# Kernel tuning notes

Measured on AMD Instinct MI355X. Metric: run time of the kernel, lower is better.

The kernel has to match this reference:

```python
import jax, jax.numpy as jnp
import numpy as np

B, N, V, D = 4, 1024, 20000, 512
DEPTH, H, DH, W = 6, 8, 64, 512
NB = N // W
NS = 512               # num_state_vectors
PM = D // 4            # dynamic pos-bias MLP width
XL_LAYERS = (4, 5)     # 0-indexed (config layers 5, 6)
REC_LAYER = 3          # 0-indexed (config layer 4)
QK_RMS = {3, 4, 5}     # recurrent + xl layers use qk rmsnorm
QK_SCALE = 8.0
FF = 4 * D


def _ln(x, g, eps=1e-5):
    mu = x.mean(-1, keepdims=True)
    var = ((x - mu) ** 2).mean(-1, keepdims=True)
    return (x - mu) * jax.lax.rsqrt(var + eps) * g


def _l2norm(x):
    return x * jax.lax.rsqrt((x * x).sum(-1, keepdims=True) + 1e-12)


def _pos_bias(pos_w1, pos_b1, pos_w2, pos_b2, pos_w3, pos_b3):
    # MLP over scalar relative distance -> per-head bias table [W, H]
    d = jnp.arange(W, dtype=jnp.float32)[:, None]
    h = jax.nn.silu(d @ pos_w1 + pos_b1)
    h = jax.nn.silu(h @ pos_w2 + pos_b2)
    table = h @ pos_w3 + pos_b3                       # [W, H]
    i = jnp.arange(W)[:, None]
    j = jnp.arange(2 * W)[None, :]
    rel = jnp.abs(i + W - j)                          # distance to key in [prev|cur] window
    win = (j > i) & (j <= i + W)                      # causal sliding window of width W
    pb = table[jnp.where(win, rel, 0)]                # [W, 2W, H]
    return jnp.transpose(pb, (2, 0, 1)), win          # [H, W, 2W], [W, 2W]


def setup_inputs() -> dict:
    key = jax.random.key(0)
    ks = iter(jax.random.split(key, 64))
    w = lambda shape, s=0.02: jax.random.normal(next(ks), shape, jnp.float32) * s
    return dict(
        x=jax.random.randint(next(ks), (B, N), 0, V, jnp.int32),
        tok_emb=w((V, D)),
        pos_w1=w((1, PM)), pos_b1=jnp.zeros((PM,), jnp.float32),
        pos_w2=w((PM, PM)), pos_b2=jnp.zeros((PM,), jnp.float32),
        pos_w3=w((PM, H)), pos_b3=jnp.zeros((H,), jnp.float32),
        ln_g=jnp.ones((DEPTH, D), jnp.float32),
        Wq=w((DEPTH, D, H * DH)), Wk=w((DEPTH, D, H * DH)),
        Wv=w((DEPTH, D, H * DH)), Wo=w((DEPTH, H * DH, D)),
        q_scale=jnp.ones((DEPTH, DH), jnp.float32),
        k_scale=jnp.ones((DEPTH, DH), jnp.float32),
        Wo_state=w((H * DH, D)),
        state_norm_g=jnp.ones((D,), jnp.float32),
        Wq2s=w((D, H * DH)), Ws2q=w((D, H * DH)), Ws2kv=w((D, 2 * DH)),
        W_state_out=w((H * DH, D)),
        ema_beta=jnp.zeros((D,), jnp.float32),
        ff_g=jnp.ones((DEPTH, D), jnp.float32),
        ff_w1=w((DEPTH, D, FF)), ff_b1=jnp.zeros((DEPTH, FF), jnp.float32),
        ff_w2=w((DEPTH, FF, D)), ff_b2=jnp.zeros((DEPTH, D), jnp.float32),
        final_g=jnp.ones((D,), jnp.float32),
        W_logits=w((D, V)),
        xl_mem_k=jax.random.normal(next(ks), (len(XL_LAYERS), B, W, H, DH), jnp.float32),
        xl_mem_v=jax.random.normal(next(ks), (len(XL_LAYERS), B, W, H, DH), jnp.float32),
        states=jax.random.normal(next(ks), (B, NS, D), jnp.float32),
    )


def reference(x, tok_emb, pos_w1, pos_b1, pos_w2, pos_b2, pos_w3, pos_b3,
              ln_g, Wq, Wk, Wv, Wo, q_scale, k_scale, Wo_state,
              state_norm_g, Wq2s, Ws2q, Ws2kv, W_state_out, ema_beta,
              ff_g, ff_w1, ff_b1, ff_w2, ff_b2, final_g, W_logits,
              xl_mem_k, xl_mem_v, states):
    pb, win = _pos_bias(pos_w1, pos_b1, pos_w2, pos_b2, pos_w3, pos_b3)
    j = jnp.arange(2 * W)
    no_mem = win & (j[None, :] >= W)                  # first block of a non-xl layer has no memory
    scale_dh = DH ** -0.5
    # enhanced recurrence: rotate the xl memory stack one layer down
    xk = jnp.roll(xl_mem_k, -1, axis=0)
    xv = jnp.roll(xl_mem_v, -1, axis=0)

    hstate = tok_emb[x]                               # [B, N, D]
    next_xl_k, next_xl_v = [], []
    next_states = states
    xl_idx = 0
    for l in range(DEPTH):
        xn = _ln(hstate, ln_g[l])
        q = (xn @ Wq[l]).reshape(B, N, H, DH)
        k = (xn @ Wk[l]).reshape(B, N, H, DH)
        v = (xn @ Wv[l]).reshape(B, N, H, DH)
        if l in QK_RMS:
            q = _l2norm(q) * q_scale[l]
            k = _l2norm(k) * k_scale[l]
            scale = QK_SCALE
        else:
            scale = scale_dh
        qb = q.reshape(B, NB, W, H, DH)
        kb = k.reshape(B, NB, W, H, DH)
        vb = v.reshape(B, NB, W, H, DH)
        is_xl = l in XL_LAYERS
        if is_xl:
            mem_k, mem_v = xk[xl_idx], xv[xl_idx]     # [B, W, H, DH] kv carried from prior call
            valid = jnp.stack([win] * NB)             # [NB, W, 2W]
        else:
            mem_k = jnp.zeros_like(kb[:, 0])
            mem_v = jnp.zeros_like(vb[:, 0])
            valid = jnp.stack([no_mem] + [win] * (NB - 1))
        # each block attends to [previous block | current block]
        pk = jnp.concatenate([mem_k[:, None], kb[:, :-1]], axis=1)
        pv = jnp.concatenate([mem_v[:, None], vb[:, :-1]], axis=1)
        kcat = jnp.concatenate([pk, kb], axis=2)      # [B, NB, 2W, H, DH]
        vcat = jnp.concatenate([pv, vb], axis=2)
        scores = jnp.einsum('bnihd,bnjhd->bnhij', qb * scale, kcat) + pb[None, None]
        scores = jnp.where(valid[None, :, None], scores, -1e9)
        attn = jax.nn.softmax(scores, axis=-1)
        out = jnp.einsum('bnhij,bnjhd->bnihd', attn, vcat).reshape(B, N, H * DH)
        branch = out @ Wo[l]
        if l == REC_LAYER:
            # recurrent state vectors: scan over blocks carrying states
            xn_blk = jnp.moveaxis(xn.reshape(B, NB, W, D), 1, 0)   # [NB, B, W, D]
            kb_s = jnp.moveaxis(kb, 1, 0)
            vb_s = jnp.moveaxis(vb, 1, 0)

            def step(st, inp):
                xb, kblk, vblk = inp
                sn = _ln(st, state_norm_g)
                s_k, s_v = jnp.split(sn @ Ws2kv, 2, axis=-1)       # single-head kv [B, NS, DH]
                # block tokens cross-attend to states
                q2s = (xb @ Wq2s).reshape(B, W, H, DH) * scale_dh
                a = jax.nn.softmax(jnp.einsum('bihd,bjd->bhij', q2s, s_k), -1)
                t_out = jnp.einsum('bhij,bjd->bihd', a, s_v).reshape(B, W, H * DH)
                # states attend to [states | block tokens]
                sq = (sn @ Ws2q).reshape(B, NS, H, DH) * scale_dh
                kc = jnp.concatenate([jnp.broadcast_to(s_k[:, :, None], (B, NS, H, DH)), kblk], axis=1)
                vc = jnp.concatenate([jnp.broadcast_to(s_v[:, :, None], (B, NS, H, DH)), vblk], axis=1)
                a2 = jax.nn.softmax(jnp.einsum('bihd,bjhd->bhij', sq, kc), -1)
                s_out = jnp.einsum('bhij,bjhd->bihd', a2, vc).reshape(B, NS, H * DH) @ W_state_out
                decay = jax.nn.sigmoid(ema_beta)
                return decay * st + (1.0 - decay) * s_out, t_out

            next_states, t_outs = jax.lax.scan(step, states, (xn_blk, kb_s, vb_s))
            to_state = jnp.moveaxis(t_outs, 0, 1).reshape(B, N, H * DH)
            branch = branch + to_state @ Wo_state
        hstate = hstate + branch
        if is_xl:
            next_xl_k.append(kb[:, -1])
            next_xl_v.append(vb[:, -1])
            xl_idx += 1
        fn = _ln(hstate, ff_g[l])
        hstate = hstate + (jax.nn.gelu(fn @ ff_w1[l] + ff_b1[l]) @ ff_w2[l] + ff_b2[l])

    logits = _ln(hstate, final_g) @ W_logits          # [B, N, V]
    return logits, jnp.stack(next_xl_k), jnp.stack(next_xl_v), next_states
```

## Files before the change

### kernel.cpp

```cpp
#include <hip/hip_runtime.h>
#include <math.h>


typedef __attribute__((ext_vector_type(8))) _Float16 f16x8;
typedef __attribute__((ext_vector_type(4))) float f32x4;

__device__ __forceinline__ ushort f2h(float f){
  _Float16 h = (_Float16)f;
  return *reinterpret_cast<ushort*>(&h);
}
__device__ __forceinline__ uint pkh2(float a, float b){
  return (uint)f2h(a) | ((uint)f2h(b)<<16);
}

__global__ __launch_bounds__(256)
void k_prep(const float* __restrict__ src, ushort* __restrict__ dh,
            int K, int N, int Npad, long zStride){
  __shared__ float tile[32][33];
  int z = blockIdx.z;
  src += (size_t)z*K*N;
  dh  += (size_t)z*zStride;
  int n0 = blockIdx.x*32, k0 = blockIdx.y*32;
  int tx = threadIdx.x&31, ty = threadIdx.x>>5;
#pragma unroll
  for (int i=0;i<4;i++){
    int kk = k0 + ty + i*8, nn = n0 + tx;
    tile[ty+i*8][tx] = (nn < N) ? src[(size_t)kk*N + nn] : 0.f;
  }
  __syncthreads();
#pragma unroll
  for (int i=0;i<4;i++){
    int nn = n0 + ty + i*8, kk = k0 + tx;
    dh[(size_t)nn*K + kk] = f2h(tile[tx][ty+i*8]);
  }
}

__global__ __launch_bounds__(256)
void k_vtrans(const float* __restrict__ src, ushort* __restrict__ dst,
              long sB, int sR, int sMH, long dB, long dH, int NK){
  __shared__ float tile[64][65];
  int kc = blockIdx.x, h = blockIdx.y, b = blockIdx.z;
  int t = threadIdx.x;
  int key = t>>2, doff = (t&3)*16;
  const float* sp = src + (size_t)b*sB + (size_t)(kc*64+key)*sR + (sMH? h*64:0) + doff;
#pragma unroll
  for (int u=0;u<4;u++){
    float4 v = *reinterpret_cast<const float4*>(sp + u*4);
    tile[key][doff+u*4+0]=v.x; tile[key][doff+u*4+1]=v.y;
    tile[key][doff+u*4+2]=v.z; tile[key][doff+u*4+3]=v.w;
  }
  __syncthreads();
  int d = t>>2, kf = (t&3)*16;
  ushort* dp = dst + (size_t)b*dB + (size_t)h*dH + (size_t)d*NK + kc*64 + kf;
  ushort tmp[16];
#pragma unroll
  for (int u=0;u<16;u++) tmp[u] = f2h(tile[kf+u][d]);
  uint4 o0 = make_uint4((uint)tmp[0]|((uint)tmp[1]<<16), (uint)tmp[2]|((uint)tmp[3]<<16),
                        (uint)tmp[4]|((uint)tmp[5]<<16), (uint)tmp[6]|((uint)tmp[7]<<16));
  uint4 o1 = make_uint4((uint)tmp[8]|((uint)tmp[9]<<16), (uint)tmp[10]|((uint)tmp[11]<<16),
                        (uint)tmp[12]|((uint)tmp[13]<<16),(uint)tmp[14]|((uint)tmp[15]<<16));
  *reinterpret_cast<uint4*>(dp)   = o0;
  *reinterpret_cast<uint4*>(dp+8) = o1;
}

__global__ __launch_bounds__(256)
void k_vtrans16(const ushort* __restrict__ src, ushort* __restrict__ dst,
                long sB, int sR, long dB, int NK){
  __shared__ ushort tile[64][72];
  int kc = blockIdx.x, b = blockIdx.z;
  int t = threadIdx.x;
  int key = t>>2, doff = (t&3)*16;
  const ushort* sp = src + (size_t)b*sB + (size_t)(kc*64+key)*sR + doff;
  *reinterpret_cast<uint4*>(&tile[key][doff])   = *reinterpret_cast<const uint4*>(sp);
  *reinterpret_cast<uint4*>(&tile[key][doff+8]) = *reinterpret_cast<const uint4*>(sp+8);
  __syncthreads();
  int d = t>>2, kf = (t&3)*16;
  ushort* dp = dst + (size_t)b*dB + (size_t)d*NK + kc*64 + kf;
  ushort tmp[16];
#pragma unroll
  for (int u=0;u<16;u++) tmp[u] = tile[kf+u][d];
  uint4 o0 = make_uint4((uint)tmp[0]|((uint)tmp[1]<<16), (uint)tmp[2]|((uint)tmp[3]<<16),
                        (uint)tmp[4]|((uint)tmp[5]<<16), (uint)tmp[6]|((uint)tmp[7]<<16));
  uint4 o1 = make_uint4((uint)tmp[8]|((uint)tmp[9]<<16), (uint)tmp[10]|((uint)tmp[11]<<16),
                        (uint)tmp[12]|((uint)tmp[13]<<16),(uint)tmp[14]|((uint)tmp[15]<<16));
  *reinterpret_cast<uint4*>(dp)   = o0;
  *reinterpret_cast<uint4*>(dp+8) = o1;
}

__global__ void k_cvt(ushort* __restrict__ dst, const float* __restrict__ src, int n2){
  int idx = blockIdx.x*blockDim.x + threadIdx.x;
  if (idx >= n2) return;
  reinterpret_cast<uint*>(dst)[idx] = pkh2(src[2*idx], src[2*idx+1]);
}

__global__ void k_embed(const int* __restrict__ x, const float* __restrict__ emb,
                        float* __restrict__ h, int total4){
  int idx = blockIdx.x*blockDim.x + threadIdx.x;
  if (idx >= total4) return;
  int row = idx >> 7;
  int c4  = idx & 127;
  int tok = x[row];
  reinterpret_cast<float4*>(h)[idx] =
      reinterpret_cast<const float4*>(emb)[(size_t)tok*128 + c4];
}

__global__ void k_postable(const float* __restrict__ w1, const float* __restrict__ b1,
                           const float* __restrict__ w2, const float* __restrict__ b2,
                           const float* __restrict__ w3, const float* __restrict__ b3,
                           float* __restrict__ table){
  __shared__ float h1[128];
  __shared__ float h2[128];
  int d = blockIdx.x, t = threadIdx.x;
  float a = (float)d * w1[t] + b1[t];
  h1[t] = a / (1.f + __expf(-a));
  __syncthreads();
  float acc = b2[t];
  for (int p=0;p<128;p++) acc += h1[p]*w2[p*128+t];
  h2[t] = acc / (1.f + __expf(-acc));
  __syncthreads();
  if (t < 8){
    float acc2 = b3[t];
    for (int p=0;p<128;p++) acc2 += h2[p]*w3[p*8+t];
    table[d*8+t] = acc2;
  }
}

__global__ void k_ln(const float* __restrict__ x, const float* __restrict__ g,
                     ushort* __restrict__ y16){
  int row = blockIdx.x;
  int t = threadIdx.x;
  float2 v = reinterpret_cast<const float2*>(x + (size_t)row*512)[t];
  float s = v.x+v.y, ss = v.x*v.x+v.y*v.y;
  for (int o=32;o;o>>=1){ s += __shfl_down(s,o); ss += __shfl_down(ss,o); }
  __shared__ float ls[4], lss[4];
  __shared__ float smu, srs;
  int wid = t>>6;
  if ((t&63)==0){ ls[wid]=s; lss[wid]=ss; }
  __syncthreads();
  if (t==0){
    float S=ls[0]+ls[1]+ls[2]+ls[3], SS=lss[0]+lss[1]+lss[2]+lss[3];
    float mu = S*(1.f/512.f);
    float var = SS*(1.f/512.f) - mu*mu;
    smu = mu; srs = rsqrtf(var + 1e-5f);
  }
  __syncthreads();
  float mu=smu, rs=srs;
  float2 gg = reinterpret_cast<const float2*>(g)[t];
  float ya = (v.x-mu)*rs*gg.x, yb = (v.y-mu)*rs*gg.y;
  *reinterpret_cast<uint*>(&y16[(size_t)row*512 + 2*t]) = pkh2(ya, yb);
}

__device__ __forceinline__ float geluf(float x){
  float u = 1.5957691216f*(x + 0.044715f*x*x*x);
  return x / (1.f + __expf(-u));
}

template<int ACC, int EPI, int OUT16>
__global__ __launch_bounds__(256)
void k_gemmh(const ushort* __restrict__ A, const ushort* __restrict__ Bt,
             const float* __restrict__ bias, float* __restrict__ C,
             ushort* __restrict__ C16, int M, int N, int K){
  __shared__ ushort As[128][68];
  __shared__ ushort Bs[128][68];
  const int t = threadIdx.x;
  const int m0 = blockIdx.x*128, n0 = blockIdx.y*128;
  const int w = t>>6, lane = t&63;
  const int wm = (w>>1)*64, wn = (w&1)*64;
  const int fr = lane&15, fg = lane>>4;
  const int srow = t>>1, sko = (t&1)*32;

  f32x4 acc[4][4];
#pragma unroll
  for (int i=0;i<4;i++)
#pragma unroll
    for (int j=0;j<4;j++){ acc[i][j][0]=0.f; acc[i][j][1]=0.f; acc[i][j][2]=0.f; acc[i][j][3]=0.f; }

  const ushort* ap = A  + (size_t)(m0+srow)*K + sko;
  const ushort* bp = Bt + (size_t)(n0+srow)*K + sko;

  for (int k0=0; k0<K; k0+=64){
    uint4 av[4], bv[4];
#pragma unroll
    for (int u=0;u<4;u++){
      av[u] = *reinterpret_cast<const uint4*>(ap + k0 + u*8);
      bv[u] = *reinterpret_cast<const uint4*>(bp + k0 + u*8);
    }
#pragma unroll
    for (int u=0;u<4;u++){
      *reinterpret_cast<uint4*>(&As[srow][sko+u*8]) = av[u];
      *reinterpret_cast<uint4*>(&Bs[srow][sko+u*8]) = bv[u];
    }
    __syncthreads();
#pragma unroll
    for (int kk=0;kk<2;kk++){
      f16x8 af[4], bf[4];
#pragma unroll
      for (int mi=0;mi<4;mi++)
        af[mi] = *reinterpret_cast<const f16x8*>(&As[wm+mi*16+fr][kk*32+fg*8]);
#pragma unroll
      for (int nj=0;nj<4;nj++)
        bf[nj] = *reinterpret_cast<const f16x8*>(&Bs[wn+nj*16+fr][kk*32+fg*8]);
#pragma unroll
      for (int mi=0;mi<4;mi++)
#pragma unroll
        for (int nj=0;nj<4;nj++)
          acc[mi][nj] = __builtin_amdgcn_mfma_f32_16x16x32_f16(af[mi], bf[nj], acc[mi][nj], 0,0,0);
    }
    __syncthreads();
  }
#pragma unroll
  for (int mi=0;mi<4;mi++){
#pragma unroll
    for (int r=0;r<4;r++){
      int row = m0 + wm + mi*16 + fg*4 + r;
#pragma unroll
      for (int nj=0;nj<4;nj++){
        int col = n0 + wn + nj*16 + fr;
        if (col < N){
          float val = acc[mi][nj][r];
          if (bias) val += bias[col];
          if (EPI==1) val = geluf(val);
          if (OUT16){
            C16[(size_t)row*N + col] = f2h(val);
          } else {
            if (ACC) C[(size_t)row*N + col] += val; else C[(size_t)row*N + col] = val;
          }
        }
      }
    }
  }
}

template<int REMAP>
__global__ __launch_bounds__(256)
void k_gemmqk(const ushort* __restrict__ A, const ushort* __restrict__ Bt,
              ushort* __restrict__ C1h, int ld1, int N1,
              ushort* __restrict__ C2h, int ld2,
              const float* __restrict__ qsc, const float* __restrict__ ksc,
              float* __restrict__ xlk,
              int nb, int M, int N, int K){
  __shared__ ushort As[128][68];
  __shared__ ushort Bs[128][68];
  const int t = threadIdx.x;
  const int m0 = blockIdx.x*128, n0 = blockIdx.y*128;
  const int w = t>>6, lane = t&63;
  const int wm = (w>>1)*64, wn = (w&1)*64;
  const int fr = lane&15, fg = lane>>4;
  const int srow = t>>1, sko = (t&1)*32;

  f32x4 acc[4][4];
#pragma unroll
  for (int i=0;i<4;i++)
#pragma unroll
    for (int j=0;j<4;j++){ acc[i][j][0]=0.f; acc[i][j][1]=0.f; acc[i][j][2]=0.f; acc[i][j][3]=0.f; }

  int mrow = m0 + srow;
  int arow = REMAP ? ((mrow>>9)*1024 + nb*512 + (mrow&511)) : mrow;
  const ushort* ap = A  + (size_t)arow*K + sko;
  const ushort* bp = Bt + (size_t)(n0+srow)*K + sko;

  for (int k0=0; k0<K; k0+=64){
    uint4 av[4], bv[4];
#pragma unroll
    for (int u=0;u<4;u++){
      av[u] = *reinterpret_cast<const uint4*>(ap + k0 + u*8);
      bv[u] = *reinterpret_cast<const uint4*>(bp + k0 + u*8);
    }
#pragma unroll
    for (int u=0;u<4;u++){
      *reinterpret_cast<uint4*>(&As[srow][sko+u*8]) = av[u];
      *reinterpret_cast<uint4*>(&Bs[srow][sko+u*8]) = bv[u];
    }
    __syncthreads();
#pragma unroll
    for (int kk=0;kk<2;kk++){
      f16x8 af[4], bf[4];
#pragma unroll
      for (int mi=0;mi<4;mi++)
        af[mi] = *reinterpret_cast<const f16x8*>(&As[wm+mi*16+fr][kk*32+fg*8]);
#pragma unroll
      for (int nj=0;nj<4;nj++)
        bf[nj] = *reinterpret_cast<const f16x8*>(&Bs[wn+nj*16+fr][kk*32+fg*8]);
#pragma unroll
      for (int mi=0;mi<4;mi++)
#pragma unroll
        for (int nj=0;nj<4;nj++)
          acc[mi][nj] = __builtin_amdgcn_mfma_f32_16x16x32_f16(af[mi], bf[nj], acc[mi][nj], 0,0,0);
    }
    __syncthreads();
  }
#pragma unroll
  for (int mi=0;mi<4;mi++){
#pragma unroll
    for (int r=0;r<4;r++){
      int row = m0 + wm + mi*16 + fg*4 + r;
      float vals[4];
#pragma unroll
      for (int nj=0;nj<4;nj++) vals[nj] = acc[mi][nj][r];
      if (qsc){
        float ss = vals[0]*vals[0]+vals[1]*vals[1]+vals[2]*vals[2]+vals[3]*vals[3];
        ss += __shfl_xor(ss,1);
        ss += __shfl_xor(ss,2);
        ss += __shfl_xor(ss,4);
        ss += __shfl_xor(ss,8);
        float rs = rsqrtf(ss + 1e-12f);
        const float* sc = ((n0+wn) < N1) ? qsc : ksc;
#pragma unroll
        for (int nj=0;nj<4;nj++) vals[nj] = vals[nj]*rs*sc[nj*16+fr];
      }
#pragma unroll
      for (int nj=0;nj<4;nj++){
        int col = n0 + wn + nj*16 + fr;
        float val = vals[nj];
        if (col < N1){
          C1h[(size_t)row*ld1 + col] = f2h(val);
        } else if (col < N){
          if (C2h) C2h[(size_t)row*ld2 + (col-N1)] = f2h(val);
          if (xlk && (row&1023) >= 512)
            xlk[((size_t)(row>>10)*512 + (row&1023) - 512)*512 + (col-N1)] = val;
        }
      }
    }
  }
}

template<int ACC, int EPI, int OUT16, int VT>
__global__ __launch_bounds__(256)
void k_gemmh64(const ushort* __restrict__ A, const ushort* __restrict__ Bt,
               const float* __restrict__ bias, float* __restrict__ C,
               ushort* __restrict__ C16, ushort* __restrict__ vT,
               float* __restrict__ xlv, int M, int N, int K){
  __shared__ ushort As[64][68];
  __shared__ ushort Bs[128][68];
  const int t = threadIdx.x;
  const int m0 = blockIdx.x*64, n0 = blockIdx.y*128;
  const int w = t>>6, lane = t&63;
  const int wm = (w>>1)*32, wn = (w&1)*64;
  const int fr = lane&15, fg = lane>>4;
  const int srowA = t>>2, skoA = (t&3)*16;
  const int srowB = t>>1, skoB = (t&1)*32;

  f32x4 acc[2][4];
#pragma unroll
  for (int i=0;i<2;i++)
#pragma unroll
    for (int j=0;j<4;j++){ acc[i][j][0]=0.f; acc[i][j][1]=0.f; acc[i][j][2]=0.f; acc[i][j][3]=0.f; }

  const ushort* ap = A  + (size_t)(m0+srowA)*K + skoA;
  const ushort* bp = Bt + (size_t)(n0+srowB)*K + skoB;

  for (int k0=0; k0<K; k0+=64){
    uint4 a0 = *reinterpret_cast<const uint4*>(ap + k0);
    uint4 a1 = *reinterpret_cast<const uint4*>(ap + k0 + 8);
    uint4 b0 = *reinterpret_cast<const uint4*>(bp + k0);
    uint4 b1 = *reinterpret_cast<const uint4*>(bp + k0 + 8);
    uint4 b2 = *reinterpret_cast<const uint4*>(bp + k0 + 16);
    uint4 b3 = *reinterpret_cast<const uint4*>(bp + k0 + 24);
    *reinterpret_cast<uint4*>(&As[srowA][skoA])    = a0;
    *reinterpret_cast<uint4*>(&As[srowA][skoA+8])  = a1;
    *reinterpret_cast<uint4*>(&Bs[srowB][skoB])    = b0;
    *reinterpret_cast<uint4*>(&Bs[srowB][skoB+8])  = b1;
    *reinterpret_cast<uint4*>(&Bs[srowB][skoB+16]) = b2;
    *reinterpret_cast<uint4*>(&Bs[srowB][skoB+24]) = b3;
    __syncthreads();
#pragma unroll
    for (int kk=0;kk<2;kk++){
      f16x8 af[2], bf[4];
#pragma unroll
      for (int mi=0;mi<2;mi++)
        af[mi] = *reinterpret_cast<const f16x8*>(&As[wm+mi*16+fr][kk*32+fg*8]);
#pragma unroll
      for (int nj=0;nj<4;nj++)
        bf[nj] = *reinterpret_cast<const f16x8*>(&Bs[wn+nj*16+fr][kk*32+fg*8]);
#pragma unroll
      for (int mi=0;mi<2;mi++)
#pragma unroll
        for (int nj=0;nj<4;nj++)
          acc[mi][nj] = __builtin_amdgcn_mfma_f32_16x16x32_f16(af[mi], bf[nj], acc[mi][nj], 0,0,0);
    }
    __syncthreads();
  }
#pragma unroll
  for (int mi=0;mi<2;mi++){
#pragma unroll
    for (int r=0;r<4;r++){
      int row = m0 + wm + mi*16 + fg*4 + r;
#pragma unroll
      for (int nj=0;nj<4;nj++){
        int col = n0 + wn + nj*16 + fr;
        if (col < N){
          float val = acc[mi][nj][r];
          if (EPI==2){
            size_t idx = (size_t)row*N + col;
            float old = C[idx];
            float dec = 1.f/(1.f+__expf(-bias[col]));
            C[idx] = dec*old + (1.f-dec)*val;
          } else {
            if (bias) val += bias[col];
            if (EPI==1) val = geluf(val);
            if (OUT16){
              if (C16) C16[(size_t)row*N + col] = f2h(val);
            } else if (C){
              if (ACC) C[(size_t)row*N + col] += val; else C[(size_t)row*N + col] = val;
            }
            if (VT && xlv && (row&1023) >= 512)
              xlv[((size_t)(row>>10)*512 + (row&1023) - 512)*512 + col] = val;
          }
        }
      }
    }
  }
  if (VT){
#pragma unroll
    for (int mi=0;mi<2;mi++)
#pragma unroll
      for (int r=0;r<4;r++)
#pragma unroll
        for (int nj=0;nj<4;nj++)
          Bs[wn+nj*16+fr][wm+mi*16+fg*4+r] = f2h(acc[mi][nj][r]);
    __syncthreads();
    int c = t>>1, half = t&1;
    int hh = (n0+c)>>6, dd = (n0+c)&63;
    int bb = m0>>10, posb = m0&1023;
    ushort* dp = vT + (size_t)bb*524288 + (size_t)hh*65536 + (size_t)dd*1024 + posb + half*32;
#pragma unroll
    for (int u=0;u<4;u++)
      *reinterpret_cast<uint4*>(dp + u*8) = *reinterpret_cast<const uint4*>(&Bs[c][half*32 + u*8]);
  }
}

__global__ __launch_bounds__(256)
void k_attn_win(const ushort* __restrict__ q16, const ushort* __restrict__ k16,
                const ushort* __restrict__ vTb,
                const ushort* __restrict__ xlK, const ushort* __restrict__ xlVT,
                int isxl, ushort* __restrict__ O, float scale,
                const float* __restrict__ table){
  __shared__ ushort Qs[64][72];
  __shared__ ushort Ks[64][72];
  __shared__ ushort Vs[64][72];
  __shared__ ushort Pw[4][16][72];
  __shared__ float tcol[512];
  const int b = blockIdx.z, h = blockIdx.y;
  const int nb = blockIdx.x>>3, qt = blockIdx.x&7;
  const int t = threadIdx.x, w = t>>6, lane = t&63;
  const int fr = lane&15, fg = lane>>4;
  tcol[t]     = table[t*8 + h];
  tcol[t+256] = table[(t+256)*8 + h];

  const ushort* Q  = q16 + (size_t)nb*262144;
  const ushort* K1 = k16 + (size_t)nb*262144;
  const ushort* V1 = vTb + (size_t)nb*512;
  ushort* Op = O + (size_t)nb*262144;
  const int has_mem = (nb==1) || isxl;
  const ushort* K0; long k0B; const ushort* V0; long vt0B, vt0H; int vt0D;
  if (nb==1){ K0=k16; k0B=524288; V0=vTb; vt0B=524288; vt0H=65536; vt0D=1024; }
  else if (isxl){ K0=xlK; k0B=262144; V0=xlVT; vt0B=262144; vt0H=32768; vt0D=512; }
  else { K0=k16; k0B=524288; V0=vTb; vt0B=524288; vt0H=65536; vt0D=1024; }

  {
    int qrow = t>>2, doff = (t&3)*16;
    const ushort* qp = Q + (size_t)b*524288 + (size_t)(qt*64+qrow)*512 + h*64 + doff;
    *reinterpret_cast<uint4*>(&Qs[qrow][doff])   = *reinterpret_cast<const uint4*>(qp);
    *reinterpret_cast<uint4*>(&Qs[qrow][doff+8]) = *reinterpret_cast<const uint4*>(qp+8);
  }
  __syncthreads();
  f16x8 aq[2];
  aq[0] = *reinterpret_cast<const f16x8*>(&Qs[w*16+fr][fg*8]);
  aq[1] = *reinterpret_cast<const f16x8*>(&Qs[w*16+fr][32+fg*8]);

  f32x4 so[4];
#pragma unroll
  for (int dt=0;dt<4;dt++){ so[dt][0]=0.f; so[dt][1]=0.f; so[dt][2]=0.f; so[dt][3]=0.f; }
  float m[4] = {-1e30f,-1e30f,-1e30f,-1e30f};
  float lsum[4] = {0.f,0.f,0.f,0.f};

  const int srow = t>>2, sdo = (t&3)*16;
  const int vd = t>>2,   vkf = (t&3)*16;

  int jt0 = has_mem ? qt : 8;
  int jt1 = qt + 8; if (jt1 > 15) jt1 = 15;

  for (int jt=jt0; jt<=jt1; jt++){
    {
      int key = jt*64 + srow;
      const ushort* kp;
      if (key < 512) kp = K0 + (size_t)b*k0B + (size_t)key*512 + h*64 + sdo;
      else           kp = K1 + (size_t)b*524288 + (size_t)(key-512)*512 + h*64 + sdo;
      *reinterpret_cast<uint4*>(&Ks[srow][sdo])   = *reinterpret_cast<const uint4*>(kp);
      *reinterpret_cast<uint4*>(&Ks[srow][sdo+8]) = *reinterpret_cast<const uint4*>(kp+8);
    }
    {
      const ushort* vp;
      if (jt*64 < 512) vp = V0 + (size_t)b*vt0B + (size_t)h*vt0H + (size_t)vd*vt0D + jt*64 + vkf;
      else             vp = V1 + (size_t)b*524288 + (size_t)h*65536 + (size_t)vd*1024 + (jt*64-512) + vkf;
      *reinterpret_cast<uint4*>(&Vs[vd][vkf])   = *reinterpret_cast<const uint4*>(vp);
      *reinterpret_cast<uint4*>(&Vs[vd][vkf+8]) = *reinterpret_cast<const uint4*>(vp+8);
    }
    __syncthreads();
    f32x4 sacc[4];
#pragma unroll
    for (int kt=0;kt<4;kt++){ sacc[kt][0]=0.f; sacc[kt][1]=0.f; sacc[kt][2]=0.f; sacc[kt][3]=0.f; }
#pragma unroll
    for (int ks=0;ks<2;ks++){
#pragma unroll
      for (int kt=0;kt<4;kt++){
        f16x8 bf = *reinterpret_cast<const f16x8*>(&Ks[kt*16+fr][ks*32+fg*8]);
        sacc[kt] = __builtin_amdgcn_mfma_f32_16x16x32_f16(aq[ks], bf, sacc[kt], 0,0,0);
      }
    }
#pragma unroll
    for (int r=0;r<4;r++){
      float sv[4];
      int ia = qt*64 + w*16 + fg*4 + r;
#pragma unroll
      for (int kt=0;kt<4;kt++){
        float s = sacc[kt][r]*scale;
        int jg = jt*64 + kt*16 + fr;
        bool valid = (jg > ia) && (jg <= ia+512) && (has_mem || jg >= 512);
        sv[kt] = valid ? s + tcol[ia+512-jg] : -1e9f;
      }
      float tm = fmaxf(fmaxf(sv[0],sv[1]), fmaxf(sv[2],sv[3]));
      tm = fmaxf(tm, __shfl_xor(tm,1));
      tm = fmaxf(tm, __shfl_xor(tm,2));
      tm = fmaxf(tm, __shfl_xor(tm,4));
      tm = fmaxf(tm, __shfl_xor(tm,8));
      float mn = fmaxf(m[r], tm);
      float c = __expf(m[r]-mn);
      m[r] = mn;
      float ps = 0.f;
#pragma unroll
      for (int kt=0;kt<4;kt++){
        float pp = (sv[kt] <= -1e8f) ? 0.f : __expf(sv[kt]-mn);
        ps += pp;
        Pw[w][fg*4+r][kt*16+fr] = f2h(pp);
      }
      ps += __shfl_xor(ps,1);
      ps += __shfl_xor(ps,2);
      ps += __shfl_xor(ps,4);
      ps += __shfl_xor(ps,8);
      lsum[r] = lsum[r]*c + ps;
#pragma unroll
      for (int dt=0;dt<4;dt++) so[dt][r] *= c;
    }
#pragma unroll
    for (int ks=0;ks<2;ks++){
      f16x8 pa = *reinterpret_cast<const f16x8*>(&Pw[w][fr][ks*32+fg*8]);
#pragma unroll
      for (int dt=0;dt<4;dt++){
        f16x8 bv = *reinterpret_cast<const f16x8*>(&Vs[dt*16+fr][ks*32+fg*8]);
        so[dt] = __builtin_amdgcn_mfma_f32_16x16x32_f16(pa, bv, so[dt], 0,0,0);
      }
    }
    __syncthreads();
  }
#pragma unroll
  for (int r=0;r<4;r++){
    int row = qt*64 + w*16 + fg*4 + r;
    float inv = 1.f / lsum[r];
    ushort* op = Op + (size_t)b*524288 + (size_t)row*512 + h*64;
#pragma unroll
    for (int dt=0;dt<4;dt++)
      op[dt*16+fr] = f2h(so[dt][r]*inv);
  }
}

__global__ __launch_bounds__(256)
void k_attn_rec(const ushort* __restrict__ q2s, const ushort* __restrict__ sq,
                const ushort* __restrict__ skv, const ushort* __restrict__ svT,
                const ushort* __restrict__ kblk, const ushort* __restrict__ vblk,
                ushort* __restrict__ ts, ushort* __restrict__ sa){
  __shared__ ushort Qs[64][72];
  __shared__ ushort Ks[64][72];
  __shared__ ushort Vs[64][72];
  __shared__ ushort Pw[4][16][72];
  const int b = blockIdx.z, h = blockIdx.y;
  const int task = blockIdx.x>>3, qt = blockIdx.x&7;
  const int t = threadIdx.x, w = t>>6, lane = t&63;
  const int fr = lane&15, fg = lane>>4;

  const ushort* Q; const ushort* K1; int k1R, k1H;
  const ushort* VT1; long vt1B, vt1H; int vt1D;
  int nt; ushort* O; long oB;
  if (task==0){
    Q=q2s; K1=skv; k1R=128; k1H=0;
    VT1=svT; vt1B=32768; vt1H=0; vt1D=512;
    nt=8; O=ts; oB=524288;
  } else {
    Q=sq; K1=kblk; k1R=512; k1H=1;
    VT1=vblk; vt1B=524288; vt1H=65536; vt1D=1024;
    nt=16; O=sa; oB=262144;
  }

  {
    int qrow = t>>2, doff = (t&3)*16;
    const ushort* qp = Q + (size_t)b*262144 + (size_t)(qt*64+qrow)*512 + h*64 + doff;
    *reinterpret_cast<uint4*>(&Qs[qrow][doff])   = *reinterpret_cast<const uint4*>(qp);
    *reinterpret_cast<uint4*>(&Qs[qrow][doff+8]) = *reinterpret_cast<const uint4*>(qp+8);
  }
  __syncthreads();
  f16x8 aq[2];
  aq[0] = *reinterpret_cast<const f16x8*>(&Qs[w*16+fr][fg*8]);
  aq[1] = *reinterpret_cast<const f16x8*>(&Qs[w*16+fr][32+fg*8]);

  f32x4 so[4];
#pragma unroll
  for (int dt=0;dt<4;dt++){ so[dt][0]=0.f; so[dt][1]=0.f; so[dt][2]=0.f; so[dt][3]=0.f; }
  float m[4] = {-1e30f,-1e30f,-1e30f,-1e30f};
  float lsum[4] = {0.f,0.f,0.f,0.f};

  const int srow = t>>2, sdo = (t&3)*16;
  const int vd = t>>2,   vkf = (t&3)*16;

  for (int jt=0; jt<nt; jt++){
    {
      int key = jt*64 + srow;
      const ushort* kp;
      if (key < 512) kp = skv + (size_t)b*65536 + (size_t)key*128 + sdo;
      else           kp = K1 + (size_t)b*524288 + (size_t)(key-512)*k1R + (k1H? h*64:0) + sdo;
      *reinterpret_cast<uint4*>(&Ks[srow][sdo])   = *reinterpret_cast<const uint4*>(kp);
      *reinterpret_cast<uint4*>(&Ks[srow][sdo+8]) = *reinterpret_cast<const uint4*>(kp+8);
    }
    {
      const ushort* vp;
      if (jt*64 < 512) vp = svT + (size_t)b*32768 + (size_t)vd*512 + jt*64 + vkf;
      else             vp = VT1 + (size_t)b*vt1B + (size_t)h*vt1H + (size_t)vd*vt1D + (jt*64-512) + vkf;
      *reinterpret_cast<uint4*>(&Vs[vd][vkf])   = *reinterpret_cast<const uint4*>(vp);
      *reinterpret_cast<uint4*>(&Vs[vd][vkf+8]) = *reinterpret_cast<const uint4*>(vp+8);
    }
    __syncthreads();
    f32x4 sacc[4];
#pragma unroll
    for (int kt=0;kt<4;kt++){ sacc[kt][0]=0.f; sacc[kt][1]=0.f; sacc[kt][2]=0.f; sacc[kt][3]=0.f; }
#pragma unroll
    for (int ks=0;ks<2;ks++){
#pragma unroll
      for (int kt=0;kt<4;kt++){
        f16x8 bf = *reinterpret_cast<const f16x8*>(&Ks[kt*16+fr][ks*32+fg*8]);
        sacc[kt] = __builtin_amdgcn_mfma_f32_16x16x32_f16(aq[ks], bf, sacc[kt], 0,0,0);
      }
    }
#pragma unroll
    for (int r=0;r<4;r++){
      float sv[4];
#pragma unroll
      for (int kt=0;kt<4;kt++) sv[kt] = sacc[kt][r]*0.125f;
      float tm = fmaxf(fmaxf(sv[0],sv[1]), fmaxf(sv[2],sv[3]));
      tm = fmaxf(tm, __shfl_xor(tm,1));
      tm = fmaxf(tm, __shfl_xor(tm,2));
      tm = fmaxf(tm, __shfl_xor(tm,4));
      tm = fmaxf(tm, __shfl_xor(tm,8));
      float mn = fmaxf(m[r], tm);
      float c = __expf(m[r]-mn);
      m[r] = mn;
      float ps = 0.f;
#pragma unroll
      for (int kt=0;kt<4;kt++){
        float pp = __expf(sv[kt]-mn);
        ps += pp;
        Pw[w][fg*4+r][kt*16+fr] = f2h(pp);
      }
      ps += __shfl_xor(ps,1);
      ps += __shfl_xor(ps,2);
      ps += __shfl_xor(ps,4);
      ps += __shfl_xor(ps,8);
      lsum[r] = lsum[r]*c + ps;
#pragma unroll
      for (int dt=0;dt<4;dt++) so[dt][r] *= c;
    }
#pragma unroll
    for (int ks=0;ks<2;ks++){
      f16x8 pa = *reinterpret_cast<const f16x8*>(&Pw[w][fr][ks*32+fg*8]);
#pragma unroll
      for (int dt=0;dt<4;dt++){
        f16x8 bv = *reinterpret_cast<const f16x8*>(&Vs[dt*16+fr][ks*32+fg*8]);
        so[dt] = __builtin_amdgcn_mfma_f32_16x16x32_f16(pa, bv, so[dt], 0,0,0);
      }
    }
    __syncthreads();
  }
#pragma unroll
  for (int r=0;r<4;r++){
    int row = qt*64 + w*16 + fg*4 + r;
    float inv = 1.f / lsum[r];
    ushort* op = O + (size_t)b*oB + (size_t)row*512 + h*64;
#pragma unroll
    for (int dt=0;dt<4;dt++)
      op[dt*16+fr] = f2h(so[dt][r]*inv);
  }
}

__global__ void k_copy(float* __restrict__ dst, const float* __restrict__ src, int n){
  int idx = blockIdx.x*blockDim.x + threadIdx.x;
  if (idx < n) dst[idx] = src[idx];
}

extern "C" void kernel_launch(void* const* d_in, const int* in_sizes, int n_in,
                              void* d_out, int out_size, void* d_ws, size_t ws_size,
                              hipStream_t stream){
  if (ws_size < (size_t)119554048) return;

  const int*   x        = (const int*)  d_in[0];
  const float* tok_emb  = (const float*)d_in[1];
  const float* pw1 = (const float*)d_in[2];
  const float* pb1 = (const float*)d_in[3];
  const float* pw2 = (const float*)d_in[4];
  const float* pb2 = (const float*)d_in[5];
  const float* pw3 = (const float*)d_in[6];
  const float* pb3 = (const float*)d_in[7];
  const float* ln_g = (const float*)d_in[8];
  const float* Wq = (const float*)d_in[9];
  const float* Wk = (const float*)d_in[10];
  const float* Wv = (const float*)d_in[11];
  const float* Wo = (const float*)d_in[12];
  const float* q_scale = (const float*)d_in[13];
  const float* k_scale = (const float*)d_in[14];
  const float* Wo_state = (const float*)d_in[15];
  const float* state_norm_g = (const float*)d_in[16];
  const float* Wq2s = (const float*)d_in[17];
  const float* Ws2q = (const float*)d_in[18];
  const float* Ws2kv = (const float*)d_in[19];
  const float* W_state_out = (const float*)d_in[20];
  const float* ema_beta = (const float*)d_in[21];
  const float* ff_g = (const float*)d_in[22];
  const float* ff_w1 = (const float*)d_in[23];
  const float* ff_b1 = (const float*)d_in[24];
  const float* ff_w2 = (const float*)d_in[25];
  const float* ff_b2 = (const float*)d_in[26];
  const float* final_g = (const float*)d_in[27];
  const float* W_logits = (const float*)d_in[28];
  const float* xl_mem_k = (const float*)d_in[29];
  const float* xl_mem_v = (const float*)d_in[30];
  const float* states_in = (const float*)d_in[31];

  float* out = (float*)d_out;
  float* out_xlk    = out + 81920000;
  float* out_xlv    = out + 84017152;
  float* out_states = out + 86114304;

  float* p = (float*)d_ws;
  float* hstate   = p; p += 2097152;
  float* states_cur = p; p += 1048576;
  float* table    = p; p += 4096;

  ushort* us = (ushort*)p;
  ushort* wqkh  = us; us += 3145728;
  ushort* wvT   = us; us += 1572864;
  ushort* woT   = us; us += 1572864;
  ushort* ffw1T = us; us += 6291456;
  ushort* ffw2T = us; us += 6291456;
  ushort* wostT = us; us += 262144;
  ushort* wstoutT = us; us += 262144;
  ushort* wq2sh = us; us += 262144;
  ushort* wsqkvh = us; us += 327680;
  ushort* wlogT  = us; us += 10289152;
  ushort* vTb   = us; us += 2097152;
  ushort* xlvT  = us; us += 2097152;
  ushort* svT   = us; us += 131072;
  ushort* xn16  = us; us += 2097152;
  ushort* ao16  = us; us += 2097152;
  ushort* ff1_16 = us; us += 8388608;
  ushort* q16   = us; us += 2097152;
  ushort* k16   = us; us += 2097152;
  ushort* xlk16 = us; us += 2097152;
  ushort* ts16   = ff1_16;
  ushort* sa16   = ff1_16 + 2097152;
  ushort* sn16   = ff1_16 + 3145728;
  ushort* sq16   = ff1_16 + 4194304;
  ushort* q2s16  = ff1_16 + 5242880;
  ushort* skv16  = ff1_16 + 6291456;

  k_prep<<<dim3(16,16,6),256,0,stream>>>(Wq, wqkh, 512,512,512, 524288);
  k_prep<<<dim3(16,16,6),256,0,stream>>>(Wk, wqkh+262144, 512,512,512, 524288);
  k_prep<<<dim3(16,16,6),256,0,stream>>>(Wv, wvT, 512,512,512, 262144);
  k_prep<<<dim3(16,16,6),256,0,stream>>>(Wo, woT, 512,512,512, 262144);
  k_prep<<<dim3(64,16,6),256,0,stream>>>(ff_w1, ffw1T, 512,2048,2048, 1048576);
  k_prep<<<dim3(16,64,6),256,0,stream>>>(ff_w2, ffw2T, 2048,512,512, 1048576);
  k_prep<<<dim3(16,16,1),256,0,stream>>>(Wo_state, wostT, 512,512,512, 262144);
  k_prep<<<dim3(16,16,1),256,0,stream>>>(W_state_out, wstoutT, 512,512,512, 262144);
  k_prep<<<dim3(16,16,1),256,0,stream>>>(Wq2s, wq2sh, 512,512,512, 262144);
  k_prep<<<dim3(16,16,1),256,0,stream>>>(Ws2q, wsqkvh, 512,512,512, 327680);
  k_prep<<<dim3(4,16,1),256,0,stream>>>(Ws2kv, wsqkvh+262144, 512,128,128, 327680);
  k_prep<<<dim3(628,16,1),256,0,stream>>>(W_logits, wlogT, 512,20000,20096, 10289152);

  for (int s=0;s<2;s++)
    k_vtrans<<<dim3(8,8,4),256,0,stream>>>(xl_mem_v + (size_t)s*1048576,
                                           xlvT + (size_t)s*1048576,
                                           262144L, 512, 1, 262144L, 32768L, 512);
  k_cvt<<<4096,256,0,stream>>>(xlk16, xl_mem_k, 1048576);

  k_embed<<<2048, 256, 0, stream>>>(x, tok_emb, hstate, 524288);
  k_postable<<<512, 128, 0, stream>>>(pw1,pb1,pw2,pb2,pw3,pb3, table);
  k_copy<<<4096, 256, 0, stream>>>(states_cur, states_in, 1048576);

  for (int l=0;l<6;l++){
    bool isxl = (l==4 || l==5);
    int xli = l-4;
    int src = (l==4)? 1 : 0;
    k_ln<<<4096,256,0,stream>>>(hstate, ln_g + l*512, xn16);
    float scale = 0.125f;
    const float* qsc = nullptr; const float* ksc = nullptr;
    if (l>=3){ qsc = q_scale + l*64; ksc = k_scale + l*64; scale = 8.f; }
    k_gemmqk<0><<<dim3(32,8),256,0,stream>>>(xn16,
        wqkh + (size_t)l*524288,
        q16, 512, 512, k16, 512, qsc, ksc,
        isxl ? out_xlk + (size_t)xli*1048576 : nullptr,
        0, 4096, 1024, 512);
    k_gemmh64<0,0,0,1><<<dim3(64,4),256,0,stream>>>(xn16, wvT + (size_t)l*262144,
        nullptr, nullptr, nullptr, vTb,
        isxl ? out_xlv + (size_t)xli*1048576 : nullptr, 4096,512,512);

    k_attn_win<<<dim3(16,8,4),256,0,stream>>>(
        q16, k16, vTb,
        isxl ? xlk16 + (size_t)src*1048576 : k16,
        isxl ? xlvT  + (size_t)src*1048576 : vTb,
        isxl ? 1 : 0, ao16, scale, table);

    k_gemmh64<1,0,0,0><<<dim3(64,4),256,0,stream>>>(ao16, woT + (size_t)l*262144,
        nullptr, hstate, nullptr, nullptr, nullptr, 4096,512,512);
    if (l==3){
      for (int nb=0;nb<2;nb++){
        k_ln<<<2048,256,0,stream>>>(states_cur, state_norm_g, sn16);
        k_gemmqk<0><<<dim3(16,5),256,0,stream>>>(sn16, wsqkvh,
            sq16, 512, 512, skv16, 128, nullptr, nullptr, nullptr, 0, 2048, 640, 512);
        k_vtrans16<<<dim3(8,1,4),256,0,stream>>>(skv16 + 64, svT, 65536L, 128, 32768L, 512);
        k_gemmqk<1><<<dim3(16,4),256,0,stream>>>(xn16, wq2sh,
            q2s16, 512, 512, nullptr, 0, nullptr, nullptr, nullptr, nb, 2048, 512, 512);
        k_attn_rec<<<dim3(16,8,4),256,0,stream>>>(
            q2s16, sq16, skv16, svT,
            k16 + (size_t)nb*262144, vTb + (size_t)nb*512,
            ts16 + (size_t)nb*262144, sa16);
        k_gemmh64<0,2,0,0><<<dim3(32,4),256,0,stream>>>(sa16, wstoutT, ema_beta,
            states_cur, nullptr, nullptr, nullptr, 2048,512,512);
      }
      k_gemmh64<1,0,0,0><<<dim3(64,4),256,0,stream>>>(ts16, wostT, nullptr,
          hstate, nullptr, nullptr, nullptr, 4096,512,512);
    }
    k_ln<<<4096,256,0,stream>>>(hstate, ff_g + l*512, xn16);
    k_gemmh<0,1,1><<<dim3(32,16),256,0,stream>>>(xn16, ffw1T + (size_t)l*1048576, ff_b1 + l*2048, nullptr, ff1_16, 4096,2048,512);
    k_gemmh64<1,0,0,0><<<dim3(64,4),256,0,stream>>>(ff1_16, ffw2T + (size_t)l*1048576, ff_b2 + l*512, hstate, nullptr, nullptr, nullptr, 4096,512,2048);
  }
  k_ln<<<4096,256,0,stream>>>(hstate, final_g, xn16);
  k_gemmh<0,0,0><<<dim3(32,157),256,0,stream>>>(xn16, wlogT, nullptr, out, nullptr, 4096,20000,512);
  k_copy<<<4096, 256, 0, stream>>>(out_states, states_cur, 1048576);
}
```

Before: 1.491 ms.

## Fuse V projection into QK GEMM and batch all weight preps into one launch

The V projection is folded into the Q/K GEMM by concatenating Wq, Wk and Wv into one interleaved weight buffer and launching a single 128x128-tile GEMM over 1536 columns. V tiles take a separate epilogue that writes the transposed fp16 V and the XL v memory through shared memory. The twelve weight-transpose launches are also merged into one descriptor-driven kernel. This removes roughly a dozen kernel launches plus one GEMM pass over xn16 per layer. In exchange the prep kernel does a serial descriptor search per block, and the V tiles now use the larger 128-row tiling.

```diff
diff --git a/kernel.cpp b/kernel.cpp
--- a/kernel.cpp
+++ b/kernel.cpp
@@ -13,25 +13,36 @@
   return (uint)f2h(a) | ((uint)f2h(b)<<16);
 }
 
+struct PrepDescs {
+  const float* src[12];
+  ushort*      dst[12];
+  int K[12], N[12], nx[12], ny[12], cnt[12];
+  long zs[12];
+};
+
 __global__ __launch_bounds__(256)
-void k_prep(const float* __restrict__ src, ushort* __restrict__ dh,
-            int K, int N, int Npad, long zStride){
+void k_prep_all(PrepDescs pd){
   __shared__ float tile[32][33];
-  int z = blockIdx.z;
-  src += (size_t)z*K*N;
-  dh  += (size_t)z*zStride;
-  int n0 = blockIdx.x*32, k0 = blockIdx.y*32;
-  int tx = threadIdx.x&31, ty = threadIdx.x>>5;
-#pragma unroll
-  for (int i=0;i<4;i++){
-    int kk = k0 + ty + i*8, nn = n0 + tx;
-    tile[ty+i*8][tx] = (nn < N) ? src[(size_t)kk*N + nn] : 0.f;
+  int bid = blockIdx.x, i = 0;
+  while (i < 11 && bid >= pd.cnt[i]){ bid -= pd.cnt[i]; i++; }
+  const int K = pd.K[i], N = pd.N[i], nx = pd.nx[i];
+  const int z = bid/(nx*pd.ny[i]);
+  const int rem = bid - z*nx*pd.ny[i];
+  const int tyy = rem/nx, txx = rem - tyy*nx;
+  const float* src = pd.src[i] + (size_t)z*K*N;
+  ushort* dh = pd.dst[i] + (size_t)z*pd.zs[i];
+  const int n0 = txx*32, k0 = tyy*32;
+  const int tx = threadIdx.x&31, ty = threadIdx.x>>5;
+#pragma unroll
+  for (int u=0;u<4;u++){
+    int kk = k0 + ty + u*8, nn = n0 + tx;
+    tile[ty+u*8][tx] = (nn < N) ? src[(size_t)kk*N + nn] : 0.f;
   }
   __syncthreads();
 #pragma unroll
-  for (int i=0;i<4;i++){
-    int nn = n0 + ty + i*8, kk = k0 + tx;
-    dh[(size_t)nn*K + kk] = f2h(tile[tx][ty+i*8]);
+  for (int u=0;u<4;u++){
+    int nn = n0 + ty + u*8, kk = k0 + tx;
+    dh[(size_t)nn*K + kk] = f2h(tile[tx][ty+u*8]);
   }
 }
 
@@ -231,16 +242,18 @@
   }
 }
 
-template<int REMAP>
+template<int REMAP, int HASV>
 __global__ __launch_bounds__(256)
 void k_gemmqk(const ushort* __restrict__ A, const ushort* __restrict__ Bt,
               ushort* __restrict__ C1h, int ld1, int N1,
               ushort* __restrict__ C2h, int ld2,
               const float* __restrict__ qsc, const float* __restrict__ ksc,
               float* __restrict__ xlk,
+              ushort* __restrict__ vT, float* __restrict__ xlv,
               int nb, int M, int N, int K){
-  __shared__ ushort As[128][68];
-  __shared__ ushort Bs[128][68];
+  __shared__ ushort sm[17408];
+  ushort (*As)[68] = (ushort(*)[68])sm;
+  ushort (*Bs)[68] = (ushort(*)[68])(sm + 8704);
   const int t = threadIdx.x;
   const int m0 = blockIdx.x*128, n0 = blockIdx.y*128;
   const int w = t>>6, lane = t&63;
@@ -289,47 +302,83 @@
     }
     __syncthreads();
   }
-#pragma unroll
-  for (int mi=0;mi<4;mi++){
-#pragma unroll
-    for (int r=0;r<4;r++){
-      int row = m0 + wm + mi*16 + fg*4 + r;
-      float vals[4];
-#pragma unroll
-      for (int nj=0;nj<4;nj++) vals[nj] = acc[mi][nj][r];
-      if (qsc){
-        float ss = vals[0]*vals[0]+vals[1]*vals[1]+vals[2]*vals[2]+vals[3]*vals[3];
-        ss += __shfl_xor(ss,1);
-        ss += __shfl_xor(ss,2);
-        ss += __shfl_xor(ss,4);
-        ss += __shfl_xor(ss,8);
-        float rs = rsqrtf(ss + 1e-12f);
-        const float* sc = ((n0+wn) < N1) ? qsc : ksc;
-#pragma unroll
-        for (int nj=0;nj<4;nj++) vals[nj] = vals[nj]*rs*sc[nj*16+fr];
-      }
-#pragma unroll
-      for (int nj=0;nj<4;nj++){
-        int col = n0 + wn + nj*16 + fr;
-        float val = vals[nj];
-        if (col < N1){
-          C1h[(size_t)row*ld1 + col] = f2h(val);
-        } else if (col < N){
-          if (C2h) C2h[(size_t)row*ld2 + (col-N1)] = f2h(val);
-          if (xlk && (row&1023) >= 512)
-            xlk[((size_t)(row>>10)*512 + (row&1023) - 512)*512 + (col-N1)] = val;
+
+  if (HASV && n0 >= 1024){
+    const int n0v = n0 - 1024;
+    if (xlv){
+#pragma unroll
+      for (int mi=0;mi<4;mi++)
+#pragma unroll
+        for (int r=0;r<4;r++){
+          int row = m0 + wm + mi*16 + fg*4 + r;
+          if ((row&1023) >= 512){
+#pragma unroll
+            for (int nj=0;nj<4;nj++){
+              int colv = n0v + wn + nj*16 + fr;
+              xlv[((size_t)(row>>10)*512 + (row&1023) - 512)*512 + colv] = acc[mi][nj][r];
+            }
+          }
         }
-      }
-    }
-  }
-}
-
-template<int ACC, int EPI, int OUT16, int VT>
+    }
+    ushort* T = sm;
+#pragma unroll
+    for (int mi=0;mi<4;mi++)
+#pragma unroll
+      for (int r=0;r<4;r++)
+#pragma unroll
+        for (int nj=0;nj<4;nj++)
+          T[(wn+nj*16+fr)*136 + (wm+mi*16+fg*4+r)] = f2h(acc[mi][nj][r]);
+    __syncthreads();
+    int ct = t>>1, half = t&1;
+    int hh = (n0v+ct)>>6, dd = (n0v+ct)&63;
+    int bb = m0>>10, posb = m0&1023;
+    ushort* dp = vT + (size_t)bb*524288 + (size_t)hh*65536 + (size_t)dd*1024 + posb + half*64;
+    const ushort* sp2 = &T[ct*136 + half*64];
+#pragma unroll
+    for (int u=0;u<8;u++)
+      *reinterpret_cast<uint4*>(dp + u*8) = *reinterpret_cast<const uint4*>(sp2 + u*8);
+  } else {
+#pragma unroll
+    for (int mi=0;mi<4;mi++){
+#pragma unroll
+      for (int r=0;r<4;r++){
+        int row = m0 + wm + mi*16 + fg*4 + r;
+        float vals[4];
+#pragma unroll
+        for (int nj=0;nj<4;nj++) vals[nj] = acc[mi][nj][r];
+        if (qsc){
+          float ss = vals[0]*vals[0]+vals[1]*vals[1]+vals[2]*vals[2]+vals[3]*vals[3];
+          ss += __shfl_xor(ss,1);
+          ss += __shfl_xor(ss,2);
+          ss += __shfl_xor(ss,4);
+          ss += __shfl_xor(ss,8);
+          float rs = rsqrtf(ss + 1e-12f);
+          const float* sc = ((n0+wn) < N1) ? qsc : ksc;
+#pragma unroll
+          for (int nj=0;nj<4;nj++) vals[nj] = vals[nj]*rs*sc[nj*16+fr];
+        }
+#pragma unroll
+        for (int nj=0;nj<4;nj++){
+          int col = n0 + wn + nj*16 + fr;
+          float val = vals[nj];
+          if (col < N1){
+            C1h[(size_t)row*ld1 + col] = f2h(val);
+          } else if (col < N && col < 1024){
+            if (C2h) C2h[(size_t)row*ld2 + (col-N1)] = f2h(val);
+            if (xlk && (row&1023) >= 512)
+              xlk[((size_t)(row>>10)*512 + (row&1023) - 512)*512 + (col-N1)] = val;
+          }
+        }
+      }
+    }
+  }
+}
+
+template<int ACC, int EPI>
 __global__ __launch_bounds__(256)
 void k_gemmh64(const ushort* __restrict__ A, const ushort* __restrict__ Bt,
                const float* __restrict__ bias, float* __restrict__ C,
-               ushort* __restrict__ C16, ushort* __restrict__ vT,
-               float* __restrict__ xlv, int M, int N, int K){
+               int M, int N, int K){
   __shared__ ushort As[64][68];
   __shared__ ushort Bs[128][68];
   const int t = threadIdx.x;
@@ -398,34 +447,11 @@
           } else {
             if (bias) val += bias[col];
             if (EPI==1) val = geluf(val);
-            if (OUT16){
-              if (C16) C16[(size_t)row*N + col] = f2h(val);
-            } else if (C){
-              if (ACC) C[(size_t)row*N + col] += val; else C[(size_t)row*N + col] = val;
-            }
-            if (VT && xlv && (row&1023) >= 512)
-              xlv[((size_t)(row>>10)*512 + (row&1023) - 512)*512 + col] = val;
+            if (ACC) C[(size_t)row*N + col] += val; else C[(size_t)row*N + col] = val;
           }
         }
       }
     }
-  }
-  if (VT){
-#pragma unroll
-    for (int mi=0;mi<2;mi++)
-#pragma unroll
-      for (int r=0;r<4;r++)
-#pragma unroll
-        for (int nj=0;nj<4;nj++)
-          Bs[wn+nj*16+fr][wm+mi*16+fg*4+r] = f2h(acc[mi][nj][r]);
-    __syncthreads();
-    int c = t>>1, half = t&1;
-    int hh = (n0+c)>>6, dd = (n0+c)&63;
-    int bb = m0>>10, posb = m0&1023;
-    ushort* dp = vT + (size_t)bb*524288 + (size_t)hh*65536 + (size_t)dd*1024 + posb + half*32;
-#pragma unroll
-    for (int u=0;u<4;u++)
-      *reinterpret_cast<uint4*>(dp + u*8) = *reinterpret_cast<const uint4*>(&Bs[c][half*32 + u*8]);
   }
 }
 
@@ -743,8 +769,7 @@
   float* table    = p; p += 4096;
 
   ushort* us = (ushort*)p;
-  ushort* wqkh  = us; us += 3145728;
-  ushort* wvT   = us; us += 1572864;
+  ushort* wqkv  = us; us += 4718592;
   ushort* woT   = us; us += 1572864;
   ushort* ffw1T = us; us += 6291456;
   ushort* ffw2T = us; us += 6291456;
@@ -769,18 +794,24 @@
   ushort* q2s16  = ff1_16 + 5242880;
   ushort* skv16  = ff1_16 + 6291456;
 
-  k_prep<<<dim3(16,16,6),256,0,stream>>>(Wq, wqkh, 512,512,512, 524288);
-  k_prep<<<dim3(16,16,6),256,0,stream>>>(Wk, wqkh+262144, 512,512,512, 524288);
-  k_prep<<<dim3(16,16,6),256,0,stream>>>(Wv, wvT, 512,512,512, 262144);
-  k_prep<<<dim3(16,16,6),256,0,stream>>>(Wo, woT, 512,512,512, 262144);
-  k_prep<<<dim3(64,16,6),256,0,stream>>>(ff_w1, ffw1T, 512,2048,2048, 1048576);
-  k_prep<<<dim3(16,64,6),256,0,stream>>>(ff_w2, ffw2T, 2048,512,512, 1048576);
-  k_prep<<<dim3(16,16,1),256,0,stream>>>(Wo_state, wostT, 512,512,512, 262144);
-  k_prep<<<dim3(16,16,1),256,0,stream>>>(W_state_out, wstoutT, 512,512,512, 262144);
-  k_prep<<<dim3(16,16,1),256,0,stream>>>(Wq2s, wq2sh, 512,512,512, 262144);
-  k_prep<<<dim3(16,16,1),256,0,stream>>>(Ws2q, wsqkvh, 512,512,512, 327680);
-  k_prep<<<dim3(4,16,1),256,0,stream>>>(Ws2kv, wsqkvh+262144, 512,128,128, 327680);
-  k_prep<<<dim3(628,16,1),256,0,stream>>>(W_logits, wlogT, 512,20000,20096, 10289152);
+  PrepDescs pd;
+  auto setd = [&](int i, const float* s, ushort* d, int K, int N, int nx, int ny, int nz, long zs){
+    pd.src[i]=s; pd.dst[i]=d; pd.K[i]=K; pd.N[i]=N; pd.nx[i]=nx; pd.ny[i]=ny;
+    pd.cnt[i]=nx*ny*nz; pd.zs[i]=zs;
+  };
+  setd(0,  Wq,          wqkv,           512,512,  16,16,6, 786432);
+  setd(1,  Wk,          wqkv+262144,    512,512,  16,16,6, 786432);
+  setd(2,  Wv,          wqkv+524288,    512,512,  16,16,6, 786432);
+  setd(3,  Wo,          woT,            512,512,  16,16,6, 262144);
+  setd(4,  ff_w1,       ffw1T,          512,2048, 64,16,6, 1048576);
+  setd(5,  ff_w2,       ffw2T,          2048,512, 16,64,6, 1048576);
+  setd(6,  Wo_state,    wostT,          512,512,  16,16,1, 262144);
+  setd(7,  W_state_out, wstoutT,        512,512,  16,16,1, 262144);
+  setd(8,  Wq2s,        wq2sh,          512,512,  16,16,1, 262144);
+  setd(9,  Ws2q,        wsqkvh,         512,512,  16,16,1, 327680);
+  setd(10, Ws2kv,       wsqkvh+262144,  512,128,  4,16,1,  327680);
+  setd(11, W_logits,    wlogT,          512,20000,628,16,1,10289152);
+  k_prep_all<<<29568,256,0,stream>>>(pd);
 
   for (int s=0;s<2;s++)
     k_vtrans<<<dim3(8,8,4),256,0,stream>>>(xl_mem_v + (size_t)s*1048576,
@@ -800,14 +831,13 @@
     float scale = 0.125f;
     const float* qsc = nullptr; const float* ksc = nullptr;
     if (l>=3){ qsc = q_scale + l*64; ksc = k_scale + l*64; scale = 8.f; }
-    k_gemmqk<0><<<dim3(32,8),256,0,stream>>>(xn16,
-        wqkh + (size_t)l*524288,
+    k_gemmqk<0,1><<<dim3(32,12),256,0,stream>>>(xn16,
+        wqkv + (size_t)l*786432,
         q16, 512, 512, k16, 512, qsc, ksc,
         isxl ? out_xlk + (size_t)xli*1048576 : nullptr,
-        0, 4096, 1024, 512);
-    k_gemmh64<0,0,0,1><<<dim3(64,4),256,0,stream>>>(xn16, wvT + (size_t)l*262144,
-        nullptr, nullptr, nullptr, vTb,
-        isxl ? out_xlv + (size_t)xli*1048576 : nullptr, 4096,512,512);
+        vTb,
+        isxl ? out_xlv + (size_t)xli*1048576 : nullptr,
+        0, 4096, 1536, 512);
 
     k_attn_win<<<dim3(16,8,4),256,0,stream>>>(
         q16, k16, vTb,
@@ -815,29 +845,31 @@
         isxl ? xlvT  + (size_t)src*1048576 : vTb,
         isxl ? 1 : 0, ao16, scale, table);
 
-    k_gemmh64<1,0,0,0><<<dim3(64,4),256,0,stream>>>(ao16, woT + (size_t)l*262144,
-        nullptr, hstate, nullptr, nullptr, nullptr, 4096,512,512);
+    k_gemmh64<1,0><<<dim3(64,4),256,0,stream>>>(ao16, woT + (size_t)l*262144,
+        nullptr, hstate, 4096,512,512);
     if (l==3){
       for (int nb=0;nb<2;nb++){
         k_ln<<<2048,256,0,stream>>>(states_cur, state_norm_g, sn16);
-        k_gemmqk<0><<<dim3(16,5),256,0,stream>>>(sn16, wsqkvh,
-            sq16, 512, 512, skv16, 128, nullptr, nullptr, nullptr, 0, 2048, 640, 512);
+        k_gemmqk<0,0><<<dim3(16,5),256,0,stream>>>(sn16, wsqkvh,
+            sq16, 512, 512, skv16, 128, nullptr, nullptr, nullptr,
+            nullptr, nullptr, 0, 2048, 640, 512);
         k_vtrans16<<<dim3(8,1,4),256,0,stream>>>(skv16 + 64, svT, 65536L, 128, 32768L, 512);
-        k_gemmqk<1><<<dim3(16,4),256,0,stream>>>(xn16, wq2sh,
-            q2s16, 512, 512, nullptr, 0, nullptr, nullptr, nullptr, nb, 2048, 512, 512);
+        k_gemmqk<1,0><<<dim3(16,4),256,0,stream>>>(xn16, wq2sh,
+            q2s16, 512, 512, nullptr, 0, nullptr, nullptr, nullptr,
+            nullptr, nullptr, nb, 2048, 512, 512);
         k_attn_rec<<<dim3(16,8,4),256,0,stream>>>(
             q2s16, sq16, skv16, svT,
             k16 + (size_t)nb*262144, vTb + (size_t)nb*512,
             ts16 + (size_t)nb*262144, sa16);
-        k_gemmh64<0,2,0,0><<<dim3(32,4),256,0,stream>>>(sa16, wstoutT, ema_beta,
-            states_cur, nullptr, nullptr, nullptr, 2048,512,512);
-      }
-      k_gemmh64<1,0,0,0><<<dim3(64,4),256,0,stream>>>(ts16, wostT, nullptr,
-          hstate, nullptr, nullptr, nullptr, 4096,512,512);
+        k_gemmh64<0,2><<<dim3(32,4),256,0,stream>>>(sa16, wstoutT, ema_beta,
+            states_cur, 2048,512,512);
+      }
+      k_gemmh64<1,0><<<dim3(64,4),256,0,stream>>>(ts16, wostT, nullptr,
+          hstate, 4096,512,512);
     }
     k_ln<<<4096,256,0,stream>>>(hstate, ff_g + l*512, xn16);
     k_gemmh<0,1,1><<<dim3(32,16),256,0,stream>>>(xn16, ffw1T + (size_t)l*1048576, ff_b1 + l*2048, nullptr, ff1_16, 4096,2048,512);
-    k_gemmh64<1,0,0,0><<<dim3(64,4),256,0,stream>>>(ff1_16, ffw2T + (size_t)l*1048576, ff_b2 + l*512, hstate, nullptr, nullptr, nullptr, 4096,512,2048);
+    k_gemmh64<1,0><<<dim3(64,4),256,0,stream>>>(ff1_16, ffw2T + (size_t)l*1048576, ff_b2 + l*512, hstate, 4096,512,2048);
   }
   k_ln<<<4096,256,0,stream>>>(hstate, final_g, xn16);
   k_gemmh<0,0,0><<<dim3(32,157),256,0,stream>>>(xn16, wlogT, nullptr, out, nullptr, 4096,20000,512);
```

New measurement: 1.610 ms. 8.0% more time.
